# Kernel optimization log

Measured on AMD Instinct MI355X. Metric: run time of the kernel, lower is better.

The kernel has to match this reference:

```python
import jax, jax.numpy as jnp
import numpy as np

A, E, O = 8, 4096, 256          # agents, envs-per-agent, obs dim
H1, H2, H3 = 1024, 1024, 512     # idims
S = 4                            # number of shared (SEPS) networks


def setup_inputs() -> dict:
    key = jax.random.key(0)
    ks = jax.random.split(key, 8)
    f32 = jnp.float32
    return {
        "x": jax.random.normal(ks[0], (A, E, O), f32),
        "W1": jax.random.normal(ks[1], (S, O, H1), f32) * (1.0 / np.sqrt(O)),
        "b1": jnp.zeros((S, H1), f32),
        "W2": jax.random.normal(ks[2], (S, H1, H2), f32) * (np.sqrt(2.0) / np.sqrt(H1)),
        "b2": jnp.zeros((S, H2), f32),
        "W3": jax.random.normal(ks[3], (S, H2, H3), f32) * (np.sqrt(2.0) / np.sqrt(H2)),
        "b3": jnp.zeros((S, H3), f32),
        "seps_idx": jax.random.randint(ks[4], (A,), 0, S, dtype=jnp.int64),
    }


def reference(x, W1, b1, W2, b2, W3, b3, seps_idx):
    # x: [A, E, O]. Each of the S nets is applied (as in the original Python
    # loop) to the full stacked input, then the per-agent output is gathered
    # by seps_idx. MLP: Linear -> ReLU -> Linear -> ReLU -> Linear.
    def mlp(w1, bb1, w2, bb2, w3, bb3):
        h = jax.nn.relu(jnp.einsum('aeo,oh->aeh', x, w1) + bb1)
        h = jax.nn.relu(jnp.einsum('aeh,hg->aeg', h, w2) + bb2)
        return jnp.einsum('aeg,gk->aek', h, w3) + bb3

    out = jax.vmap(mlp)(W1, b1, W2, b2, W3, b3)           # [S, A, E, H3]
    sel = out[seps_idx, jnp.arange(A)]                    # [A, E, H3]
    return sel
```

## Files before the change

### kernel.cpp

```cpp
#include <hip/hip_runtime.h>
#include <hip/hip_bf16.h>


typedef unsigned short u16;
typedef __bf16 bf16x8 __attribute__((ext_vector_type(8)));
typedef float floatx4 __attribute__((ext_vector_type(4)));
typedef unsigned short ushort8 __attribute__((ext_vector_type(8)));

__device__ __forceinline__ u16 f2bf(float f) {
    union { float f; unsigned int u; } v; v.f = f;
    unsigned int u = v.u;
    return (u16)((u + 0x7FFFu + ((u >> 16) & 1u)) >> 16);
}

__device__ __forceinline__ void load16(const void* g, void* l) {
    __builtin_amdgcn_global_load_lds(
        (const __attribute__((address_space(1))) void*)(unsigned long long)g,
        (__attribute__((address_space(3))) void*)(unsigned int)(unsigned long long)l,
        16, 0, 0);
}

__global__ __launch_bounds__(256) void prep(
    const float* __restrict__ x, u16* __restrict__ xb,
    const float* __restrict__ W1, u16* __restrict__ w1t,
    const float* __restrict__ W2, u16* __restrict__ w2t,
    const float* __restrict__ W3, u16* __restrict__ w3t) {
    __shared__ float tile[32][33];
    int b = blockIdx.x;
    const int tid = threadIdx.x;
    if (b < 8192) {
        int i = (b * 256 + tid) * 4;
        float4 v = *(const float4*)(x + i);
        ushort4 o;
        o.x = f2bf(v.x); o.y = f2bf(v.y); o.z = f2bf(v.z); o.w = f2bf(v.w);
        *(ushort4*)(xb + i) = o;
        return;
    }
    b -= 8192;
    const float* src; u16* dst; int K, N, n0, k0, s;
    if (b < 1024) {
        s = b >> 8; int r = b & 255;
        K = 256; N = 1024; n0 = (r & 31) * 32; k0 = (r >> 5) * 32;
        src = W1; dst = w1t;
    } else if (b < 5120) {
        b -= 1024; s = b >> 10; int r = b & 1023;
        K = 1024; N = 1024; n0 = (r & 31) * 32; k0 = (r >> 5) * 32;
        src = W2; dst = w2t;
    } else {
        b -= 5120; s = b >> 9; int r = b & 511;
        K = 1024; N = 512; n0 = (r & 15) * 32; k0 = (r >> 4) * 32;
        src = W3; dst = w3t;
    }
    src += (size_t)s * K * N;
    dst += (size_t)s * N * K;
    const int tx = tid & 31, ty = tid >> 5;
#pragma unroll
    for (int j = 0; j < 32; j += 8)
        tile[ty + j][tx] = src[(size_t)(k0 + ty + j) * N + (n0 + tx)];
    __syncthreads();
#pragma unroll
    for (int j = 0; j < 32; j += 8)
        dst[(size_t)(n0 + ty + j) * K + (k0 + tx)] = f2bf(tile[tx][ty + j]);
}

template <int K, int N, bool RELU, bool OUT_BF16>
__global__ __launch_bounds__(256) void gemm_mlp(
    const u16* __restrict__ Amat, const u16* __restrict__ Wt,
    const float* __restrict__ bias, const int* __restrict__ seps,
    void* __restrict__ outp) {
    constexpr int BM = 128, BN = 128, BK = 64;
    constexpr int NNB = N / 128;
    constexpr int LNB = (NNB == 8) ? 3 : 2;
    constexpr int EW = 132;
    __shared__ float4 ldsbuf[2048];
    u16* smA = (u16*)ldsbuf;
    u16* smB = (u16*)ldsbuf + 8192;
    float* eps = (float*)ldsbuf;

    const int tid = threadIdx.x;
    const int wave = tid >> 6, lane = tid & 63;
    const int wm = wave >> 1, wn = wave & 1;
    const int quad = lane >> 4, l16 = lane & 15;

    const int bidx = blockIdx.x;
    const int t = bidx >> 3;
    const int mb = (t >> LNB) * 8 + (bidx & 7);
    const int nb = t & (NNB - 1);
    const int m0 = mb * BM;
    const int n0 = nb * BN;

    const int s = seps[m0 >> 12];
    const u16* Ab = Amat + (size_t)m0 * K;
    const u16* Bb = Wt + ((size_t)s * N + n0) * K;

    const int srow = lane >> 3;
    const int sk = ((lane & 7) ^ (lane >> 3)) * 8;

    floatx4 acc[4][4];
#pragma unroll
    for (int i = 0; i < 4; ++i)
#pragma unroll
        for (int j = 0; j < 4; ++j) acc[i][j] = (floatx4){0.f, 0.f, 0.f, 0.f};

    for (int k0 = 0; k0 < K; k0 += BK) {
#pragma unroll
        for (int j = 0; j < 4; ++j) {
            const int c = wave * 4 + j;
            const int row = c * 8 + srow;
            load16(Ab + (size_t)row * K + k0 + sk, &smA[c * 512]);
            load16(Bb + (size_t)row * K + k0 + sk, &smB[c * 512]);
        }
        __syncthreads();

#pragma unroll
        for (int h = 0; h < 2; ++h) {
            const int slot = ((h * 4 + quad) ^ (l16 & 7)) * 8;
            bf16x8 af[4], bfv[4];
#pragma unroll
            for (int t2 = 0; t2 < 4; ++t2) {
                af[t2]  = *(const bf16x8*)&smA[(wm * 64 + t2 * 16 + l16) * 64 + slot];
                bfv[t2] = *(const bf16x8*)&smB[(wn * 64 + t2 * 16 + l16) * 64 + slot];
            }
#pragma unroll
            for (int mt = 0; mt < 4; ++mt)
#pragma unroll
                for (int nt = 0; nt < 4; ++nt)
                    acc[mt][nt] = __builtin_amdgcn_mfma_f32_16x16x32_bf16(
                        af[mt], bfv[nt], acc[mt][nt], 0, 0, 0);
        }
        __syncthreads();
    }

    float bv[4];
#pragma unroll
    for (int nt = 0; nt < 4; ++nt)
        bv[nt] = bias[s * N + n0 + wn * 64 + nt * 16 + l16];

    const int rr = tid >> 4;
    const int cg = tid & 15;

#pragma unroll
    for (int mt = 0; mt < 4; ++mt) {
#pragma unroll
        for (int nt = 0; nt < 4; ++nt) {
#pragma unroll
            for (int r2 = 0; r2 < 4; ++r2) {
                float v = acc[mt][nt][r2] + bv[nt];
                if (RELU) v = fmaxf(v, 0.0f);
                eps[(wm * 16 + quad * 4 + r2) * EW + wn * 64 + nt * 16 + l16] = v;
            }
        }
        __syncthreads();
#pragma unroll
        for (int p = 0; p < 2; ++p) {
            const int lrow = p * 16 + rr;
            const int grow = m0 + ((lrow < 16) ? (mt * 16 + lrow)
                                               : (64 + mt * 16 + (lrow - 16)));
            const float* src = eps + lrow * EW + cg * 8;
            float4 v0 = *(const float4*)(src);
            float4 v1 = *(const float4*)(src + 4);
            if (OUT_BF16) {
                ushort8 o;
                o[0] = f2bf(v0.x); o[1] = f2bf(v0.y); o[2] = f2bf(v0.z); o[3] = f2bf(v0.w);
                o[4] = f2bf(v1.x); o[5] = f2bf(v1.y); o[6] = f2bf(v1.z); o[7] = f2bf(v1.w);
                *(ushort8*)((u16*)outp + (size_t)grow * N + n0 + cg * 8) = o;
            } else {
                float* dst = (float*)outp + (size_t)grow * N + n0 + cg * 8;
                *(float4*)dst = v0;
                *(float4*)(dst + 4) = v1;
            }
        }
        __syncthreads();
    }
}

extern "C" void kernel_launch(void* const* d_in, const int* in_sizes, int n_in,
                              void* d_out, int out_size, void* d_ws, size_t ws_size,
                              hipStream_t stream) {
    const float* x  = (const float*)d_in[0];
    const float* W1 = (const float*)d_in[1];
    const float* b1 = (const float*)d_in[2];
    const float* W2 = (const float*)d_in[3];
    const float* b2 = (const float*)d_in[4];
    const float* W3 = (const float*)d_in[5];
    const float* b3 = (const float*)d_in[6];
    const int* seps = (const int*)d_in[7];

    char* ws = (char*)d_ws;
    u16* w1t = (u16*)(ws);
    u16* w2t = (u16*)(ws + (2ull << 20));
    u16* w3t = (u16*)(ws + (10ull << 20));
    u16* xb  = (u16*)(ws + (14ull << 20));
    u16* h1  = (u16*)(ws + (30ull << 20));
    u16* h2  = (u16*)(ws + (94ull << 20));

    prep<<<15360, 256, 0, stream>>>(x, xb, W1, w1t, W2, w2t, W3, w3t);

    gemm_mlp<256, 1024, true, true><<<2048, 256, 0, stream>>>(xb, w1t, b1, seps, h1);
    gemm_mlp<1024, 1024, true, true><<<2048, 256, 0, stream>>>(h1, w2t, b2, seps, h2);
    gemm_mlp<1024, 512, false, false><<<1024, 256, 0, stream>>>(h2, w3t, b3, seps, d_out);
}
```

Measured before the change: 307.4 us.

## Double-buffer LDS tiles in GEMM and simplify block-to-tile mapping

The GEMM main loop now uses two LDS buffers: the next K-tile's global-to-LDS loads are issued before the current tile's MFMAs run, and one barrier per iteration replaces two. The goal is to hide global load latency behind compute. LDS use doubles to 64KB per block, which may lower occupancy. The launch also changes from a swizzled 1D grid to a plain 2D grid (M blocks on x, N blocks on y), which drops the grouping meant for L2 reuse.

Result: faster. 290.9 us (-5.4%).

```diff
diff --git a/kernel.cpp b/kernel.cpp
--- a/kernel.cpp
+++ b/kernel.cpp
@@ -69,26 +69,18 @@
     const float* __restrict__ bias, const int* __restrict__ seps,
     void* __restrict__ outp) {
     constexpr int BM = 128, BN = 128, BK = 64;
-    constexpr int NNB = N / 128;
-    constexpr int LNB = (NNB == 8) ? 3 : 2;
+    constexpr int NIT = K / BK;
     constexpr int EW = 132;
-    __shared__ float4 ldsbuf[2048];
-    u16* smA = (u16*)ldsbuf;
-    u16* smB = (u16*)ldsbuf + 8192;
-    float* eps = (float*)ldsbuf;
+    __shared__ u16 lds[4 * 8192];
+    float* eps = (float*)lds;
 
     const int tid = threadIdx.x;
     const int wave = tid >> 6, lane = tid & 63;
     const int wm = wave >> 1, wn = wave & 1;
     const int quad = lane >> 4, l16 = lane & 15;
 
-    const int bidx = blockIdx.x;
-    const int t = bidx >> 3;
-    const int mb = (t >> LNB) * 8 + (bidx & 7);
-    const int nb = t & (NNB - 1);
-    const int m0 = mb * BM;
-    const int n0 = nb * BN;
-
+    const int m0 = blockIdx.x * BM;
+    const int n0 = blockIdx.y * BN;
     const int s = seps[m0 >> 12];
     const u16* Ab = Amat + (size_t)m0 * K;
     const u16* Bb = Wt + ((size_t)s * N + n0) * K;
@@ -102,16 +94,29 @@
 #pragma unroll
         for (int j = 0; j < 4; ++j) acc[i][j] = (floatx4){0.f, 0.f, 0.f, 0.f};
 
-    for (int k0 = 0; k0 < K; k0 += BK) {
-#pragma unroll
-        for (int j = 0; j < 4; ++j) {
-            const int c = wave * 4 + j;
-            const int row = c * 8 + srow;
-            load16(Ab + (size_t)row * K + k0 + sk, &smA[c * 512]);
-            load16(Bb + (size_t)row * K + k0 + sk, &smB[c * 512]);
-        }
+#pragma unroll
+    for (int j = 0; j < 4; ++j) {
+        const int c = wave * 4 + j;
+        const int row = c * 8 + srow;
+        load16(Ab + (size_t)row * K + sk, &lds[c * 512]);
+        load16(Bb + (size_t)row * K + sk, &lds[8192 + c * 512]);
+    }
+
+    for (int it = 0; it < NIT; ++it) {
         __syncthreads();
-
+        if (it + 1 < NIT) {
+            const int k0 = (it + 1) * BK;
+            u16* dstb = &lds[((it + 1) & 1) * 16384];
+#pragma unroll
+            for (int j = 0; j < 4; ++j) {
+                const int c = wave * 4 + j;
+                const int row = c * 8 + srow;
+                load16(Ab + (size_t)row * K + k0 + sk, dstb + c * 512);
+                load16(Bb + (size_t)row * K + k0 + sk, dstb + 8192 + c * 512);
+            }
+        }
+        const u16* smA = &lds[(it & 1) * 16384];
+        const u16* smB = smA + 8192;
 #pragma unroll
         for (int h = 0; h < 2; ++h) {
             const int slot = ((h * 4 + quad) ^ (l16 & 7)) * 8;
@@ -128,8 +133,8 @@
                     acc[mt][nt] = __builtin_amdgcn_mfma_f32_16x16x32_bf16(
                         af[mt], bfv[nt], acc[mt][nt], 0, 0, 0);
         }
-        __syncthreads();
-    }
+    }
+    __syncthreads();
 
     float bv[4];
 #pragma unroll
@@ -196,7 +201,7 @@
 
     prep<<<15360, 256, 0, stream>>>(x, xb, W1, w1t, W2, w2t, W3, w3t);
 
-    gemm_mlp<256, 1024, true, true><<<2048, 256, 0, stream>>>(xb, w1t, b1, seps, h1);
-    gemm_mlp<1024, 1024, true, true><<<2048, 256, 0, stream>>>(h1, w2t, b2, seps, h2);
-    gemm_mlp<1024, 512, false, false><<<1024, 256, 0, stream>>>(h2, w3t, b3, seps, d_out);
-}
+    gemm_mlp<256, 1024, true, true><<<dim3(256, 8), 256, 0, stream>>>(xb, w1t, b1, seps, h1);
+    gemm_mlp<1024, 1024, true, true><<<dim3(256, 8), 256, 0, stream>>>(h1, w2t, b2, seps, h2);
+    gemm_mlp<1024, 512, false, false><<<dim3(256, 4), 256, 0, stream>>>(h2, w3t, b3, seps, d_out);
+}
```
